# Performance work log

Measured on AMD Instinct MI355X. Metric: run time of the kernel, lower is better.

The kernel has to match this reference:

```python
import jax, jax.numpy as jnp
import numpy as np

LEFT = 16
RIGHT = 0

def setup_inputs() -> dict:
    key = jax.random.key(0)
    k1, k2, k3, k4 = jax.random.split(key, 4)
    B, T, D = 8, 1024, 512
    Dq, Dv = 512, 512
    scale = 1.0 / np.sqrt(D)
    return {
        "inputs": jax.random.normal(k1, (B, T, D), dtype=jnp.float32),
        "M": jax.random.normal(k2, (D, Dq), dtype=jnp.float32) * scale,
        "C": jax.random.normal(k3, (D, Dq), dtype=jnp.float32) * scale,
        "V": jax.random.normal(k4, (D, Dv), dtype=jnp.float32) * scale,
    }

def _history(x, left, right):
    # x: [B, T, D] -> [B, T, W, D], window covers offsets -(left-1)..right,
    # zero-padded outside the sequence (original pads with zeros, no masking).
    B, T, D = x.shape
    offsets = jnp.arange(-(left - 1), right + 1)            # [W]
    pos = jnp.arange(T)[:, None] + offsets[None, :]         # [T, W]
    valid = (pos >= 0) & (pos < T)                          # [T, W]
    pos_c = jnp.clip(pos, 0, T - 1)
    hist = x[:, pos_c]                                      # [B, T, W, D]
    return jnp.where(valid[None, :, :, None], hist, 0.0)

def reference(inputs, M, C, V):
    # queries/keys/values projections
    queries = inputs @ M                                    # [B, T, Dq]
    keys = _history(inputs @ C, LEFT, RIGHT)                # [B, T, W, Dq]
    values = _history(inputs @ V, LEFT, RIGHT)              # [B, T, W, Dv]
    # local attention over window (no logit normalization, matching defaults)
    logits = jnp.einsum('btd,btwd->btw', queries, keys)     # [B, T, W]
    scores = jax.nn.softmax(logits, axis=-1)
    answer = jnp.einsum('btw,btwd->btd', scores, values)    # [B, T, Dv]
    # merge == 'concatenate'
    return jnp.concatenate([inputs, answer], axis=-1)
```

## Files before the change

kernel.cpp:

```cpp
#include <hip/hip_runtime.h>
#include <math.h>

constexpr int Tn = 1024;
constexpr int Dn = 512;
constexpr int BT = 8192;
constexpr int WIN = 16;

typedef short bs8 __attribute__((ext_vector_type(8)));
typedef short sh4 __attribute__((ext_vector_type(4)));
typedef unsigned short us8 __attribute__((ext_vector_type(8)));
typedef float fx4 __attribute__((ext_vector_type(4)));

__device__ inline unsigned short f2bf(float f) {
    unsigned int u = __float_as_uint(f);
    u += 0x7FFFu + ((u >> 16) & 1u);
    return (unsigned short)(u >> 16);
}
__device__ inline float bf2f(unsigned short h) {
    return __uint_as_float(((unsigned int)h) << 16);
}
__device__ inline int fsw(int m) { return (m & 3) ^ ((m >> 2) & 3); }

__global__ __launch_bounds__(256) void wprep(
    const float* __restrict__ Mw, const float* __restrict__ Cw,
    const float* __restrict__ Vw,
    float* __restrict__ Gp, short* __restrict__ Bt)
{
    __shared__ float smem[64 * 65];
    const int blk = blockIdx.x;
    const int tid = threadIdx.x;

    if (blk < 512) {
        float* As = smem;
        float* Bs = smem + 64 * 17;
        const int kch = blk >> 6;
        const int r6 = blk & 63;
        const int b0 = (r6 & 7) * 64;
        const int a0 = (r6 >> 3) * 64;
        const int tx = tid & 15, ty = tid >> 4;

        float acc[4][4] = {};
        for (int j0 = kch * 64; j0 < kch * 64 + 64; j0 += 16) {
            const int r = tid >> 2;
            const int c = (tid & 3) * 4;
            const float4 a = *(const float4*)(Mw + (size_t)(a0 + r) * Dn + j0 + c);
            As[r * 17 + c + 0] = a.x; As[r * 17 + c + 1] = a.y;
            As[r * 17 + c + 2] = a.z; As[r * 17 + c + 3] = a.w;
            const float4 b = *(const float4*)(Cw + (size_t)(b0 + r) * Dn + j0 + c);
            Bs[r * 17 + c + 0] = b.x; Bs[r * 17 + c + 1] = b.y;
            Bs[r * 17 + c + 2] = b.z; Bs[r * 17 + c + 3] = b.w;
            __syncthreads();
            #pragma unroll
            for (int kk = 0; kk < 16; ++kk) {
                float av[4], bv[4];
                #pragma unroll
                for (int i = 0; i < 4; ++i) av[i] = As[(ty * 4 + i) * 17 + kk];
                #pragma unroll
                for (int j = 0; j < 4; ++j) bv[j] = Bs[(tx * 4 + j) * 17 + kk];
                #pragma unroll
                for (int i = 0; i < 4; ++i)
                    #pragma unroll
                    for (int j = 0; j < 4; ++j)
                        acc[i][j] += av[i] * bv[j];
            }
            __syncthreads();
        }
        #pragma unroll
        for (int j = 0; j < 4; ++j) {
            const int b = b0 + tx * 4 + j;
            float4 col = make_float4(acc[0][j], acc[1][j], acc[2][j], acc[3][j]);
            *(float4*)(Gp + ((size_t)kch * 512 + b) * 512 + a0 + ty * 4) = col;
        }
    } else {
        float* tile = smem;
        const int z = blk - 512;
        const int k0 = (z & 7) * 64;
        const int n0 = (z >> 3) * 64;
        #pragma unroll
        for (int rr = 0; rr < 4; ++rr) {
            const int row = (tid >> 4) * 4 + rr;
            const int col = (tid & 15) * 4;
            const float4 w = *(const float4*)(Vw + (size_t)(k0 + row) * Dn + n0 + col);
            tile[row * 65 + col + 0] = w.x; tile[row * 65 + col + 1] = w.y;
            tile[row * 65 + col + 2] = w.z; tile[row * 65 + col + 3] = w.w;
        }
        __syncthreads();
        const int n  = tid >> 2;
        const int ks = (tid & 3) * 16;
        union { bs8 v; unsigned short u[8]; } hi0, hi1;
        #pragma unroll
        for (int i = 0; i < 8; ++i) {
            hi0.u[i] = f2bf(tile[(ks + i) * 65 + n]);
            hi1.u[i] = f2bf(tile[(ks + 8 + i) * 65 + n]);
        }
        short* base = Bt + (size_t)(512 + n0 + n) * 1024 + k0 + ks;
        *(bs8*)base       = hi0.v;
        *(bs8*)(base + 8) = hi1.v;
    }
}

__global__ __launch_bounds__(256) void pack_g(const float* __restrict__ Gp,
                                              short* __restrict__ Bt)
{
    const int i = blockIdx.x * 256 + threadIdx.x;
    const int b = i >> 6;
    const int a8 = (i & 63) * 8;
    float s[8] = {};
    #pragma unroll
    for (int kc = 0; kc < 8; ++kc) {
        const float* p = Gp + ((size_t)kc * 512 + b) * 512 + a8;
        const float4 p0 = *(const float4*)p;
        const float4 p1 = *(const float4*)(p + 4);
        s[0] += p0.x; s[1] += p0.y; s[2] += p0.z; s[3] += p0.w;
        s[4] += p1.x; s[5] += p1.y; s[6] += p1.z; s[7] += p1.w;
    }
    union { bs8 v; unsigned short u[8]; } hi, lo;
    #pragma unroll
    for (int j = 0; j < 8; ++j) {
        const unsigned short h = f2bf(s[j]);
        hi.u[j] = h;
        lo.u[j] = f2bf(s[j] - bf2f(h));
    }
    short* base = Bt + (size_t)b * 1024 + a8;
    *(bs8*)base         = hi.v;
    *(bs8*)(base + 512) = lo.v;
}

__global__ __launch_bounds__(512, 4) void gemm_mfma(
    const float* __restrict__ X, const short* __restrict__ Bt,
    short* __restrict__ Yh, short* __restrict__ Yl, short* __restrict__ Vt)
{
    __shared__ short lds[2][4][128 * 32];

    const int lin = blockIdx.x;
    const int xcd = lin & 7;
    const int s   = lin >> 3;
    int mt, nt;
    if (s < 32) {
        mt = xcd * 8 + (s & 7);
        nt = s >> 3;
    } else {
        const int v = s - 32;
        mt = xcd * 8 + (v & 7);
        nt = 4 + (v >> 3);
    }
    const int m0 = mt * 128, n0g = nt * 128;
    const int slab = nt >> 2;

    const int tid = threadIdx.x;
    const int ln  = tid & 63;
    const int wid = tid >> 6;
    const int wr = wid >> 2, wc = wid & 3;
    const int lrow = ln & 15;
    const int lkb  = ln >> 4;

    fx4 acc[4][2] = {};

    const int ar = tid >> 2;
    const int aj = tid & 3;
    const int aoff = ar * 32 + (aj ^ fsw(ar)) * 8;
    const float* xrow = X + (size_t)(m0 + ar) * 512 + aj * 8;

    const int bnr = tid >> 2, bjj = tid & 3;
    const int bjs = bjj ^ fsw(bnr);
    const size_t bsrc = (size_t)(n0g + bnr) * 1024 + bjs * 8;

    auto stageB = [&](int bi, int k0) {
        __builtin_amdgcn_global_load_lds(
            (const __attribute__((address_space(1))) unsigned int*)(Bt + bsrc + k0),
            (__attribute__((address_space(3))) unsigned int*)(&lds[bi][2][tid * 8]), 16, 0, 0);
        if (slab == 0)
            __builtin_amdgcn_global_load_lds(
                (const __attribute__((address_space(1))) unsigned int*)(Bt + bsrc + 512 + k0),
                (__attribute__((address_space(3))) unsigned int*)(&lds[bi][3][tid * 8]), 16, 0, 0);
    };
    auto writeA = [&](int bi, const float4& f0, const float4& f1) {
        const float xs[8] = {f0.x, f0.y, f0.z, f0.w, f1.x, f1.y, f1.z, f1.w};
        union { bs8 v; unsigned short u[8]; } hi, lo;
        #pragma unroll
        for (int e = 0; e < 8; ++e) {
            const unsigned short h = f2bf(xs[e]);
            hi.u[e] = h;
            lo.u[e] = f2bf(xs[e] - bf2f(h));
        }
        *(bs8*)(&lds[bi][0][aoff]) = hi.v;
        if (slab == 0) *(bs8*)(&lds[bi][1][aoff]) = lo.v;
    };
    auto compute = [&](int bi) {
        bs8 ah[4], al[4], b0[2], b1[2];
        #pragma unroll
        for (int mf = 0; mf < 4; ++mf) {
            const int m = wr * 64 + mf * 16 + lrow;
            const int off = m * 32 + ((lkb ^ fsw(m)) * 8);
            ah[mf] = *(const bs8*)(&lds[bi][0][off]);
            if (slab == 0) al[mf] = *(const bs8*)(&lds[bi][1][off]);
        }
        #pragma unroll
        for (int nf = 0; nf < 2; ++nf) {
            const int n = wc * 32 + nf * 16 + lrow;
            const int off = n * 32 + ((lkb ^ fsw(n)) * 8);
            b0[nf] = *(const bs8*)(&lds[bi][2][off]);
            if (slab == 0) b1[nf] = *(const bs8*)(&lds[bi][3][off]);
        }
        #pragma unroll
        for (int mf = 0; mf < 4; ++mf)
            #pragma unroll
            for (int nf = 0; nf < 2; ++nf) {
                acc[mf][nf] = __builtin_amdgcn_mfma_f32_16x16x32_bf16(
                    ah[mf], b0[nf], acc[mf][nf], 0, 0, 0);
                if (slab == 0) {
                    acc[mf][nf] = __builtin_amdgcn_mfma_f32_16x16x32_bf16(
                        al[mf], b0[nf], acc[mf][nf], 0, 0, 0);
                    acc[mf][nf] = __builtin_amdgcn_mfma_f32_16x16x32_bf16(
                        ah[mf], b1[nf], acc[mf][nf], 0, 0, 0);
                }
            }
    };

    {
        const float4 f0 = *(const float4*)xrow;
        const float4 f1 = *(const float4*)(xrow + 4);
        stageB(0, 0);
        writeA(0, f0, f1);
    }
    __syncthreads();

    for (int it = 0; it < 16; ++it) {
        const int bi = it & 1;
        float4 n0, n1;
        if (it < 15) {
            const float* p = xrow + (it + 1) * 32;
            n0 = *(const float4*)p;
            n1 = *(const float4*)(p + 4);
            stageB(bi ^ 1, (it + 1) * 32);
        }
        compute(bi);
        if (it < 15) writeA(bi ^ 1, n0, n1);
        __syncthreads();
    }

    if (slab == 0) {
        #pragma unroll
        for (int mf = 0; mf < 4; ++mf) {
            #pragma unroll
            for (int nf = 0; nf < 2; ++nf) {
                const int col = n0g + wc * 32 + nf * 16 + lrow;
                #pragma unroll
                for (int r = 0; r < 4; ++r) {
                    const int row = m0 + wr * 64 + mf * 16 + lkb * 4 + r;
                    const float v = acc[mf][nf][r];
                    const unsigned short h = f2bf(v);
                    Yh[(size_t)row * 512 + col] = (short)h;
                    Yl[(size_t)row * 512 + col] = (short)f2bf(v - bf2f(h));
                }
            }
        }
    } else {
        #pragma unroll
        for (int mf = 0; mf < 4; ++mf) {
            #pragma unroll
            for (int nf = 0; nf < 2; ++nf) {
                const int c = (n0g - 512) + wc * 32 + nf * 16 + lrow;
                const int row0 = m0 + wr * 64 + mf * 16 + lkb * 4;
                sh4 v4;
                #pragma unroll
                for (int r = 0; r < 4; ++r) v4[r] = (short)f2bf(acc[mf][nf][r]);
                *(sh4*)(Vt + (size_t)c * 8192 + row0) = v4;
            }
        }
    }
}

__global__ __launch_bounds__(64) void attn_mfma(
    const float* __restrict__ X,
    const short* __restrict__ Yh, const short* __restrict__ Yl,
    const short* __restrict__ Vt, float* __restrict__ out)
{
    __shared__ short Plds[16 * 32];

    const int lin = blockIdx.x;
    const int strip = (lin & 7) * 64 + (lin >> 3);
    const int t0 = strip * 16;
    const int bat = t0 >> 10;
    const int tt0 = t0 & 1023;
    const int l  = threadIdx.x;
    const int lr = l & 15;
    const int lg = l >> 4;

    const size_t yrow = (size_t)(t0 + lr) * 512 + lg * 8;
    const int srcl0 = tt0 - 15 + lr;
    const int srcl1 = tt0 + 1 + lr;
    const int r0c = srcl0 < 0 ? 0 : srcl0;
    const int r1c = srcl1 > 1023 ? 1023 : srcl1;
    const size_t xrow0 = ((size_t)(bat * 1024 + r0c)) * 512 + lg * 8;
    const size_t xrow1 = ((size_t)(bat * 1024 + r1c)) * 512 + lg * 8;

    fx4 s0a = {0,0,0,0}, s0b = {0,0,0,0};
    fx4 s1a = {0,0,0,0}, s1b = {0,0,0,0};
    #pragma unroll
    for (int k0 = 0; k0 < 512; k0 += 32) {
        const bs8 ah = *(const bs8*)(Yh + yrow + k0);
        const bs8 al = *(const bs8*)(Yl + yrow + k0);
        const float4 p0a = *(const float4*)(X + xrow0 + k0);
        const float4 p0b = *(const float4*)(X + xrow0 + k0 + 4);
        const float4 p1a = *(const float4*)(X + xrow1 + k0);
        const float4 p1b = *(const float4*)(X + xrow1 + k0 + 4);
        const float x0s[8] = {p0a.x,p0a.y,p0a.z,p0a.w,p0b.x,p0b.y,p0b.z,p0b.w};
        const float x1s[8] = {p1a.x,p1a.y,p1a.z,p1a.w,p1b.x,p1b.y,p1b.z,p1b.w};
        union { bs8 v; unsigned short u[8]; } bh0, bl0, bh1, bl1;
        #pragma unroll
        for (int e = 0; e < 8; ++e) {
            unsigned short h = f2bf(x0s[e]);
            bh0.u[e] = h; bl0.u[e] = f2bf(x0s[e] - bf2f(h));
            h = f2bf(x1s[e]);
            bh1.u[e] = h; bl1.u[e] = f2bf(x1s[e] - bf2f(h));
        }
        s0a = __builtin_amdgcn_mfma_f32_16x16x32_bf16(ah, bh0.v, s0a, 0, 0, 0);
        s0b = __builtin_amdgcn_mfma_f32_16x16x32_bf16(al, bh0.v, s0b, 0, 0, 0);
        s0b = __builtin_amdgcn_mfma_f32_16x16x32_bf16(ah, bl0.v, s0b, 0, 0, 0);
        s1a = __builtin_amdgcn_mfma_f32_16x16x32_bf16(ah, bh1.v, s1a, 0, 0, 0);
        s1b = __builtin_amdgcn_mfma_f32_16x16x32_bf16(al, bh1.v, s1b, 0, 0, 0);
        s1b = __builtin_amdgcn_mfma_f32_16x16x32_bf16(ah, bl1.v, s1b, 0, 0, 0);

        if (lr == 15) {
            float* o = out + (size_t)t0 * 1024 + k0 + lg * 8;
            *(float4*)o       = p0a;
            *(float4*)(o + 4) = p0b;
        } else {
            float* o = out + (size_t)(t0 + 1 + lr) * 1024 + k0 + lg * 8;
            *(float4*)o       = p1a;
            *(float4*)(o + 4) = p1b;
        }
    }

    #pragma unroll
    for (int r = 0; r < 4; ++r) {
        const int i = lg * 4 + r;
        const int d0 = lr - i;
        const int d1 = lr + 16 - i;
        const bool in0 = (d0 >= 0) && (d0 <= 15);
        const bool in1 = (d1 >= 0) && (d1 <= 15);
        const bool z0 = srcl0 < 0;
        float v0 = z0 ? 0.0f : (s0a[r] + s0b[r]);
        float v1 = s1a[r] + s1b[r];
        v0 = in0 ? v0 : -3.0e38f;
        v1 = in1 ? v1 : -3.0e38f;
        float m = fmaxf(v0, v1);
        #pragma unroll
        for (int st = 1; st < 16; st <<= 1) m = fmaxf(m, __shfl_xor(m, st, 64));
        const float e0 = in0 ? __expf(v0 - m) : 0.0f;
        const float e1 = in1 ? __expf(v1 - m) : 0.0f;
        float den = e0 + e1;
        #pragma unroll
        for (int st = 1; st < 16; st <<= 1) den += __shfl_xor(den, st, 64);
        const float inv = 1.0f / den;
        const float p0 = (in0 && !z0) ? e0 * inv : 0.0f;
        const float p1 = in1 ? e1 * inv : 0.0f;
        Plds[i * 32 + lr]      = (short)f2bf(p0);
        Plds[i * 32 + lr + 16] = (short)f2bf(p1);
    }
    __syncthreads();

    const bs8 pa = *(const bs8*)(Plds + lr * 32 + lg * 8);
    const long svt = (long)bat * 1024 + (tt0 - 15 + lg * 8);
    #pragma unroll
    for (int nf = 0; nf < 32; ++nf) {
        const int d = nf * 16 + lr;
        const bs8 bv = *(const bs8*)(Vt + (long)d * 8192 + svt);
        fx4 c = {0, 0, 0, 0};
        c = __builtin_amdgcn_mfma_f32_16x16x32_bf16(pa, bv, c, 0, 0, 0);
        #pragma unroll
        for (int r = 0; r < 4; ++r)
            out[(size_t)(t0 + lg * 4 + r) * 1024 + 512 + d] = c[r];
    }
}

extern "C" void kernel_launch(void* const* d_in, const int* in_sizes, int n_in,
                              void* d_out, int out_size, void* d_ws, size_t ws_size,
                              hipStream_t stream)
{
    const float* X  = (const float*)d_in[0];
    const float* Mw = (const float*)d_in[1];
    const float* Cw = (const float*)d_in[2];
    const float* Vw = (const float*)d_in[3];
    float* out = (float*)d_out;

    short* Bt = (short*)d_ws;
    float* Gp = (float*)(Bt + (size_t)1024 * 1024);
    short* Yh = (short*)(Gp + (size_t)8 * 512 * 512);
    short* Yl = Yh + (size_t)BT * 512;
    short* Vt = Yl + (size_t)BT * 512;

    wprep<<<576, 256, 0, stream>>>(Mw, Cw, Vw, Gp, Bt);
    pack_g<<<128, 256, 0, stream>>>(Gp, Bt);
    gemm_mfma<<<512, 512, 0, stream>>>(X, Bt, Yh, Yl, Vt);
    attn_mfma<<<512, 64, 0, stream>>>(X, Yh, Yl, Vt, out);
}
```

Baseline: 67.14 us.

## Split weight prep finer, software-pipeline GEMM loads, prefetch V in attention

Weight-product prep now splits K into 16 chunks instead of 8, doubling block count for more parallelism, and pack_g sums the extra partials. The GEMM main loop is restructured into a two-deep register/LDS prefetch with explicit waitcnt and sched barriers, and the slab conditionals on B/A-lo staging are removed so all slabs load both halves. The attention kernel preloads all 32 V fragments into registers up front to overlap with the logit computation. The trade-offs are extra Gp traffic, extra loads in slabs that never use the low halves, and much higher register pressure in attention.

Measured after the change: 69.27 us. 3.2% more time.

```diff
diff --git a/kernel.cpp b/kernel.cpp
--- a/kernel.cpp
+++ b/kernel.cpp
@@ -30,7 +30,7 @@
     const int blk = blockIdx.x;
     const int tid = threadIdx.x;
 
-    if (blk < 512) {
+    if (blk < 1024) {
         float* As = smem;
         float* Bs = smem + 64 * 17;
         const int kch = blk >> 6;
@@ -40,7 +40,7 @@
         const int tx = tid & 15, ty = tid >> 4;
 
         float acc[4][4] = {};
-        for (int j0 = kch * 64; j0 < kch * 64 + 64; j0 += 16) {
+        for (int j0 = kch * 32; j0 < kch * 32 + 32; j0 += 16) {
             const int r = tid >> 2;
             const int c = (tid & 3) * 4;
             const float4 a = *(const float4*)(Mw + (size_t)(a0 + r) * Dn + j0 + c);
@@ -73,7 +73,7 @@
         }
     } else {
         float* tile = smem;
-        const int z = blk - 512;
+        const int z = blk - 1024;
         const int k0 = (z & 7) * 64;
         const int n0 = (z >> 3) * 64;
         #pragma unroll
@@ -107,7 +107,7 @@
     const int a8 = (i & 63) * 8;
     float s[8] = {};
     #pragma unroll
-    for (int kc = 0; kc < 8; ++kc) {
+    for (int kc = 0; kc < 16; ++kc) {
         const float* p = Gp + ((size_t)kc * 512 + b) * 512 + a8;
         const float4 p0 = *(const float4*)p;
         const float4 p1 = *(const float4*)(p + 4);
@@ -169,10 +169,9 @@
         __builtin_amdgcn_global_load_lds(
             (const __attribute__((address_space(1))) unsigned int*)(Bt + bsrc + k0),
             (__attribute__((address_space(3))) unsigned int*)(&lds[bi][2][tid * 8]), 16, 0, 0);
-        if (slab == 0)
-            __builtin_amdgcn_global_load_lds(
-                (const __attribute__((address_space(1))) unsigned int*)(Bt + bsrc + 512 + k0),
-                (__attribute__((address_space(3))) unsigned int*)(&lds[bi][3][tid * 8]), 16, 0, 0);
+        __builtin_amdgcn_global_load_lds(
+            (const __attribute__((address_space(1))) unsigned int*)(Bt + bsrc + 512 + k0),
+            (__attribute__((address_space(3))) unsigned int*)(&lds[bi][3][tid * 8]), 16, 0, 0);
     };
     auto writeA = [&](int bi, const float4& f0, const float4& f1) {
         const float xs[8] = {f0.x, f0.y, f0.z, f0.w, f1.x, f1.y, f1.z, f1.w};
@@ -184,7 +183,7 @@
             lo.u[e] = f2bf(xs[e] - bf2f(h));
         }
         *(bs8*)(&lds[bi][0][aoff]) = hi.v;
-        if (slab == 0) *(bs8*)(&lds[bi][1][aoff]) = lo.v;
+        *(bs8*)(&lds[bi][1][aoff]) = lo.v;
     };
     auto compute = [&](int bi) {
         bs8 ah[4], al[4], b0[2], b1[2];
@@ -217,27 +216,49 @@
             }
     };
 
-    {
-        const float4 f0 = *(const float4*)xrow;
-        const float4 f1 = *(const float4*)(xrow + 4);
-        stageB(0, 0);
-        writeA(0, f0, f1);
-    }
-    __syncthreads();
-
-    for (int it = 0; it < 16; ++it) {
-        const int bi = it & 1;
-        float4 n0, n1;
-        if (it < 15) {
-            const float* p = xrow + (it + 1) * 32;
-            n0 = *(const float4*)p;
-            n1 = *(const float4*)(p + 4);
-            stageB(bi ^ 1, (it + 1) * 32);
-        }
-        compute(bi);
-        if (it < 15) writeA(bi ^ 1, n0, n1);
-        __syncthreads();
-    }
+    float4 xr0[2], xr1[2];
+    stageB(0, 0);
+    xr0[0] = *(const float4*)(xrow);
+    xr1[0] = *(const float4*)(xrow + 4);
+    xr0[1] = *(const float4*)(xrow + 32);
+    xr1[1] = *(const float4*)(xrow + 36);
+    asm volatile("s_waitcnt vmcnt(2)" ::: "memory");
+    __builtin_amdgcn_sched_barrier(0);
+    writeA(0, xr0[0], xr1[0]);
+    asm volatile("s_waitcnt lgkmcnt(0)" ::: "memory");
+    __builtin_amdgcn_sched_barrier(0);
+    __builtin_amdgcn_s_barrier();
+
+    #pragma unroll 2
+    for (int it = 0; it < 14; ++it) {
+        const int cur = it & 1, nxt = cur ^ 1;
+        stageB(nxt, (it + 1) * 32);
+        {
+            const float* p = xrow + (it + 2) * 32;
+            xr0[cur] = *(const float4*)p;
+            xr1[cur] = *(const float4*)(p + 4);
+        }
+        asm volatile("s_waitcnt vmcnt(4)" ::: "memory");
+        __builtin_amdgcn_sched_barrier(0);
+        writeA(nxt, xr0[nxt], xr1[nxt]);
+        compute(cur);
+        asm volatile("s_waitcnt lgkmcnt(0)" ::: "memory");
+        __builtin_amdgcn_sched_barrier(0);
+        asm volatile("s_waitcnt vmcnt(2)" ::: "memory");
+        __builtin_amdgcn_sched_barrier(0);
+        __builtin_amdgcn_s_barrier();
+    }
+    stageB(1, 15 * 32);
+    asm volatile("s_waitcnt vmcnt(2)" ::: "memory");
+    __builtin_amdgcn_sched_barrier(0);
+    writeA(1, xr0[1], xr1[1]);
+    compute(0);
+    asm volatile("s_waitcnt lgkmcnt(0)" ::: "memory");
+    __builtin_amdgcn_sched_barrier(0);
+    asm volatile("s_waitcnt vmcnt(0)" ::: "memory");
+    __builtin_amdgcn_sched_barrier(0);
+    __builtin_amdgcn_s_barrier();
+    compute(1);
 
     if (slab == 0) {
         #pragma unroll
@@ -271,7 +292,7 @@
     }
 }
 
-__global__ __launch_bounds__(64) void attn_mfma(
+__global__ __launch_bounds__(64, 1) void attn_mfma(
     const float* __restrict__ X,
     const short* __restrict__ Yh, const short* __restrict__ Yl,
     const short* __restrict__ Vt, float* __restrict__ out)
@@ -286,6 +307,12 @@
     const int l  = threadIdx.x;
     const int lr = l & 15;
     const int lg = l >> 4;
+
+    const long svt = (long)bat * 1024 + (tt0 - 15 + lg * 8);
+    bs8 bv[32];
+    #pragma unroll
+    for (int nf = 0; nf < 32; ++nf)
+        bv[nf] = *(const bs8*)(Vt + (long)(nf * 16 + lr) * 8192 + svt);
 
     const size_t yrow = (size_t)(t0 + lr) * 512 + lg * 8;
     const int srcl0 = tt0 - 15 + lr;
@@ -362,13 +389,11 @@
     __syncthreads();
 
     const bs8 pa = *(const bs8*)(Plds + lr * 32 + lg * 8);
-    const long svt = (long)bat * 1024 + (tt0 - 15 + lg * 8);
     #pragma unroll
     for (int nf = 0; nf < 32; ++nf) {
         const int d = nf * 16 + lr;
-        const bs8 bv = *(const bs8*)(Vt + (long)d * 8192 + svt);
         fx4 c = {0, 0, 0, 0};
-        c = __builtin_amdgcn_mfma_f32_16x16x32_bf16(pa, bv, c, 0, 0, 0);
+        c = __builtin_amdgcn_mfma_f32_16x16x32_bf16(pa, bv[nf], c, 0, 0, 0);
         #pragma unroll
         for (int r = 0; r < 4; ++r)
             out[(size_t)(t0 + lg * 4 + r) * 1024 + 512 + d] = c[r];
@@ -387,11 +412,11 @@
 
     short* Bt = (short*)d_ws;
     float* Gp = (float*)(Bt + (size_t)1024 * 1024);
-    short* Yh = (short*)(Gp + (size_t)8 * 512 * 512);
+    short* Yh = (short*)(Gp + (size_t)16 * 512 * 512);
     short* Yl = Yh + (size_t)BT * 512;
     short* Vt = Yl + (size_t)BT * 512;
 
-    wprep<<<576, 256, 0, stream>>>(Mw, Cw, Vw, Gp, Bt);
+    wprep<<<1088, 256, 0, stream>>>(Mw, Cw, Vw, Gp, Bt);
     pack_g<<<128, 256, 0, stream>>>(Gp, Bt);
     gemm_mfma<<<512, 512, 0, stream>>>(X, Bt, Yh, Yl, Vt);
     attn_mfma<<<512, 64, 0, stream>>>(X, Yh, Yl, Vt, out);
```
